# Kernel optimization log

Hardware: AMD Instinct MI355X
Metric: run time of the kernel (lower is better)

## Reference

```python
import jax, jax.numpy as jnp
import numpy as np

B, S, DIM, H = 2, 2048, 1024, 16
HD = DIM // H  # 64


def _rope(x, cos, sin):
    # x: [B, S, H, HD]; cos/sin: [S, HD//2]
    xr = x[..., 0::2]  # interleaved pairs -> real part
    xi = x[..., 1::2]  # imag part
    c = cos[None, :, None, :]
    s = sin[None, :, None, :]
    out_r = xr * c - xi * s
    out_i = xr * s + xi * c
    # re-interleave: stack on new last axis then flatten pairs
    out = jnp.stack([out_r, out_i], axis=-1).reshape(x.shape)
    return out.astype(x.dtype)


def setup_inputs() -> dict:
    key = jax.random.key(0)
    ks = jax.random.split(key, 6)
    x = jax.random.normal(ks[0], (B, S, DIM), dtype=jnp.float32)
    scale = 1.0 / np.sqrt(DIM)
    wq = jax.random.normal(ks[1], (DIM, DIM), dtype=jnp.float32) * scale
    wk = jax.random.normal(ks[2], (DIM, DIM), dtype=jnp.float32) * scale
    wv = jax.random.normal(ks[3], (DIM, DIM), dtype=jnp.float32) * scale
    wo = jax.random.normal(ks[4], (DIM, DIM), dtype=jnp.float32) * scale
    # RoPE frequencies (theta = 10000)
    inv_freq = 1.0 / (10000.0 ** (np.arange(0, HD, 2, dtype=np.float32) / HD))
    t = np.arange(S, dtype=np.float32)
    angles = np.outer(t, inv_freq)  # [S, HD//2]
    freqs_cos = jnp.asarray(np.cos(angles), dtype=jnp.float32)
    freqs_sin = jnp.asarray(np.sin(angles), dtype=jnp.float32)
    # additive causal mask [S, S]
    neg = jnp.full((S, S), -1e9, dtype=jnp.float32)
    mask = jnp.triu(neg, k=1)
    return {"x": x, "wq": wq, "wk": wk, "wv": wv, "wo": wo,
            "freqs_cos": freqs_cos, "freqs_sin": freqs_sin, "mask": mask}


def reference(x, wq, wk, wv, wo, freqs_cos, freqs_sin, mask):
    b, s, _ = x.shape
    # nn.Linear with weight W computes x @ W.T
    xq = (x @ wq.T).reshape(b, s, H, HD)
    xk = (x @ wk.T).reshape(b, s, H, HD)
    xv = (x @ wv.T).reshape(b, s, H, HD)
    xq = _rope(xq, freqs_cos, freqs_sin)
    xk = _rope(xk, freqs_cos, freqs_sin)
    # [B, H, S, S] scores, fully materialized as in the original
    scores = jnp.einsum('bqhd,bkhd->bhqk', xq, xk) / jnp.sqrt(jnp.float32(HD))
    scores = scores + mask[None, None, :, :]
    probs = jax.nn.softmax(scores.astype(jnp.float32), axis=-1).astype(xq.dtype)
    out = jnp.einsum('bhqk,bkhd->bqhd', probs, xv).reshape(b, s, DIM)
    return out @ wo.T
```

## Files before the change

kernel.cpp:

```cpp
#include <hip/hip_runtime.h>
#include <cstdint>
#include <cstddef>

typedef unsigned short u16;
typedef short bf16x8 __attribute__((ext_vector_type(8)));
typedef float f32x4 __attribute__((ext_vector_type(4)));
typedef float f32x16 __attribute__((ext_vector_type(16)));
typedef unsigned u32x2 __attribute__((ext_vector_type(2)));
typedef unsigned u32x4 __attribute__((ext_vector_type(4)));

#define NBATCH 2
#define NS 2048
#define NDIM 1024
#define NH 16
#define NHD 64

__device__ __forceinline__ u16 f2b(float f) {
  union { float f; unsigned u; } x; x.f = f;
  return (u16)((x.u + 0x7fffu + ((x.u >> 16) & 1u)) >> 16);
}

__device__ __forceinline__ unsigned cvtpk_bf16(float lo, float hi) {
  unsigned r;
  asm("v_cvt_pk_bf16_f32 %0, %1, %2" : "=v"(r) : "v"(lo), "v"(hi));
  return r;
}

__global__ void cvt_all(const float* __restrict__ x,  const float* __restrict__ wq,
                        const float* __restrict__ wk, const float* __restrict__ wv,
                        const float* __restrict__ wo,
                        u16* __restrict__ xb,  u16* __restrict__ wqb,
                        u16* __restrict__ wkb, u16* __restrict__ wvb,
                        u16* __restrict__ wob) {
  int i4 = (blockIdx.x * blockDim.x + threadIdx.x) * 4;
  const float* s; u16* d; int off;
  if (i4 < 4194304) { s = x; d = xb; off = i4; }
  else {
    int j = i4 - 4194304;
    int seg = j >> 20; off = j & 1048575;
    s = seg == 0 ? wq : seg == 1 ? wk : seg == 2 ? wv : wo;
    d = seg == 0 ? wqb : seg == 1 ? wkb : seg == 2 ? wvb : wob;
  }
  float4 v = *reinterpret_cast<const float4*>(s + off);
  ushort4 o;
  o.x = f2b(v.x); o.y = f2b(v.y); o.z = f2b(v.z); o.w = f2b(v.w);
  *reinterpret_cast<ushort4*>(d + off) = o;
}

template<int MODE>
__global__ __launch_bounds__(256, 2)
void gemm_bt(const u16* __restrict__ A, const u16* __restrict__ Bt,
             float* __restrict__ Cf, u16* __restrict__ Cb) {
  __shared__ __align__(16) u16 sA[128 * 32];
  __shared__ __align__(16) u16 sB[128 * 32];
  const int lane = threadIdx.x & 63;
  const int wid  = threadIdx.x >> 6;
  const int wm = wid >> 1, wn = wid & 1;
  const int tm = blockIdx.x * 128, tn = blockIdx.y * 128;
  const int fr = lane & 15, fq = lane >> 4;
  const int sr = lane >> 2, sc = lane & 3;

  const f32x4 fzero = {0.f, 0.f, 0.f, 0.f};
  f32x4 acc[4][4];
#pragma unroll
  for (int i = 0; i < 4; ++i)
#pragma unroll
    for (int j = 0; j < 4; ++j) acc[i][j] = fzero;

  const u16* gA0 = A  + (size_t)(tm + wid * 32 + sr) * NDIM + sc * 8;
  const u16* gB0 = Bt + (size_t)(tn + wid * 32 + sr) * NDIM + sc * 8;
  u16* lA = &sA[wid * 32 * 32];
  u16* lB = &sB[wid * 32 * 32];

  for (int k0 = 0; k0 < NDIM; k0 += 32) {
    __builtin_amdgcn_global_load_lds((const __attribute__((address_space(1))) unsigned*)(gA0 + k0),
                                     (__attribute__((address_space(3))) unsigned*)lA, 16, 0, 0);
    __builtin_amdgcn_global_load_lds((const __attribute__((address_space(1))) unsigned*)(gA0 + k0 + 16 * NDIM),
                                     (__attribute__((address_space(3))) unsigned*)(lA + 16 * 32), 16, 0, 0);
    __builtin_amdgcn_global_load_lds((const __attribute__((address_space(1))) unsigned*)(gB0 + k0),
                                     (__attribute__((address_space(3))) unsigned*)lB, 16, 0, 0);
    __builtin_amdgcn_global_load_lds((const __attribute__((address_space(1))) unsigned*)(gB0 + k0 + 16 * NDIM),
                                     (__attribute__((address_space(3))) unsigned*)(lB + 16 * 32), 16, 0, 0);
    __syncthreads();

    bf16x8 af[4], bff[4];
#pragma unroll
    for (int i = 0; i < 4; ++i)
      af[i] = *reinterpret_cast<const bf16x8*>(&sA[(wm * 64 + i * 16 + fr) * 32 + fq * 8]);
#pragma unroll
    for (int i = 0; i < 4; ++i)
      bff[i] = *reinterpret_cast<const bf16x8*>(&sB[(wn * 64 + i * 16 + fr) * 32 + fq * 8]);
#pragma unroll
    for (int mi = 0; mi < 4; ++mi)
#pragma unroll
      for (int ni = 0; ni < 4; ++ni)
        acc[mi][ni] = __builtin_amdgcn_mfma_f32_16x16x32_bf16(af[mi], bff[ni], acc[mi][ni], 0, 0, 0);
    __syncthreads();
  }

#pragma unroll
  for (int mi = 0; mi < 4; ++mi) {
#pragma unroll
    for (int ni = 0; ni < 4; ++ni) {
#pragma unroll
      for (int r = 0; r < 4; ++r) {
        const int row = tm + wm * 64 + mi * 16 + fq * 4 + r;
        const int col = tn + wn * 64 + ni * 16 + fr;
        float val = acc[mi][ni][r];
        if (MODE == 0) {
          Cf[(size_t)row * NDIM + col] = val;
        } else {
          const int hh = row >> 6, d = row & 63;
          const int b = col >> 11, s = col & (NS - 1);
          Cb[((size_t)(b * NH + hh) * NHD + d) * NS + s] = f2b(val);
        }
      }
    }
  }
}

__global__ __launch_bounds__(256, 2)
void gemm_qk(const u16* __restrict__ A, const u16* __restrict__ WQ, const u16* __restrict__ WK,
             u16* __restrict__ Qo, u16* __restrict__ Ko,
             const float* __restrict__ cosp, const float* __restrict__ sinp) {
  __shared__ __align__(16) u16 sA[128 * 32];
  __shared__ __align__(16) u16 sB[128 * 32];
  const int lane = threadIdx.x & 63;
  const int wid  = threadIdx.x >> 6;
  const int wm = wid >> 1, wn = wid & 1;
  const int tnG = blockIdx.y * 128;
  const int which = tnG >> 10;
  const u16* Bt = which ? WK : WQ;
  u16* Cb = which ? Ko : Qo;
  const int tm = blockIdx.x * 128, tn = tnG & 1023;
  const int fr = lane & 15, fq = lane >> 4;
  const int sr = lane >> 2, sc = lane & 3;

  const f32x4 fzero = {0.f, 0.f, 0.f, 0.f};
  f32x4 acc[4][4];
#pragma unroll
  for (int i = 0; i < 4; ++i)
#pragma unroll
    for (int j = 0; j < 4; ++j) acc[i][j] = fzero;

  const u16* gA0 = A  + (size_t)(tm + wid * 32 + sr) * NDIM + sc * 8;
  const u16* gB0 = Bt + (size_t)(tn + wid * 32 + sr) * NDIM + sc * 8;
  u16* lA = &sA[wid * 32 * 32];
  u16* lB = &sB[wid * 32 * 32];

  for (int k0 = 0; k0 < NDIM; k0 += 32) {
    __builtin_amdgcn_global_load_lds((const __attribute__((address_space(1))) unsigned*)(gA0 + k0),
                                     (__attribute__((address_space(3))) unsigned*)lA, 16, 0, 0);
    __builtin_amdgcn_global_load_lds((const __attribute__((address_space(1))) unsigned*)(gA0 + k0 + 16 * NDIM),
                                     (__attribute__((address_space(3))) unsigned*)(lA + 16 * 32), 16, 0, 0);
    __builtin_amdgcn_global_load_lds((const __attribute__((address_space(1))) unsigned*)(gB0 + k0),
                                     (__attribute__((address_space(3))) unsigned*)lB, 16, 0, 0);
    __builtin_amdgcn_global_load_lds((const __attribute__((address_space(1))) unsigned*)(gB0 + k0 + 16 * NDIM),
                                     (__attribute__((address_space(3))) unsigned*)(lB + 16 * 32), 16, 0, 0);
    __syncthreads();

    bf16x8 af[4], bff[4];
#pragma unroll
    for (int i = 0; i < 4; ++i)
      af[i] = *reinterpret_cast<const bf16x8*>(&sA[(wm * 64 + i * 16 + fr) * 32 + fq * 8]);
#pragma unroll
    for (int i = 0; i < 4; ++i)
      bff[i] = *reinterpret_cast<const bf16x8*>(&sB[(wn * 64 + i * 16 + fr) * 32 + fq * 8]);
#pragma unroll
    for (int mi = 0; mi < 4; ++mi)
#pragma unroll
      for (int ni = 0; ni < 4; ++ni)
        acc[mi][ni] = __builtin_amdgcn_mfma_f32_16x16x32_bf16(af[mi], bff[ni], acc[mi][ni], 0, 0, 0);
    __syncthreads();
  }

#pragma unroll
  for (int mi = 0; mi < 4; ++mi) {
#pragma unroll
    for (int ni = 0; ni < 4; ++ni) {
#pragma unroll
      for (int r = 0; r < 4; ++r) {
        const int row = tm + wm * 64 + mi * 16 + fq * 4 + r;
        const int col = tn + wn * 64 + ni * 16 + fr;
        float val = acc[mi][ni][r];
        const int b = row >> 11, s = row & (NS - 1);
        const int h = col >> 6,  d = col & 63;
        const int fi = d >> 1;
        const float c  = cosp[s * 32 + fi];
        const float sn = sinp[s * 32 + fi];
        const float partner = __shfl_xor(val, 1);
        val = (d & 1) ? (partner * sn + val * c) : (val * c - partner * sn);
        Cb[((size_t)(b * NH + h) * NS + s) * NHD + d] = f2b(val);
      }
    }
  }
}

__global__ __launch_bounds__(256, 2)
void attn_fwd(const u16* __restrict__ Q, const u16* __restrict__ K,
              const u16* __restrict__ Vt, u16* __restrict__ O) {
  __shared__ __align__(16) u16 t_lds[4][32 * 68];
  const int lane = threadIdx.x & 63;
  const int w = threadIdx.x >> 6;
  const int bh  = blockIdx.x & 31;
  const int grp = 15 - (int)(blockIdx.x >> 5);
  const int q0w = grp * 128 + w * 32;
  const int qc = lane & 31, hi = lane >> 5;
  const size_t baseQ = (size_t)bh * NS * NHD;
  const size_t baseV = (size_t)bh * NHD * NS;
  const int qrow = q0w + qc;

  bf16x8 qf[4];
#pragma unroll
  for (int s = 0; s < 4; ++s)
    qf[s] = *reinterpret_cast<const bf16x8*>(&Q[baseQ + (size_t)qrow * NHD + s * 16 + hi * 8]);

  f32x16 oA = {}, oB = {};
  float m = -1e30f, l = 0.f;

  const int nkt = (q0w + 95) >> 6;
  for (int kt = 0; kt < nkt; ++kt) {
    const int key0 = kt * 64;
    bf16x8 kf0[4], kf1[4], vf0[4], vf1[4];
#pragma unroll
    for (int s = 0; s < 4; ++s) {
      kf0[s] = *reinterpret_cast<const bf16x8*>(&K[baseQ + (size_t)(key0 + qc) * NHD + s * 16 + hi * 8]);
      kf1[s] = *reinterpret_cast<const bf16x8*>(&K[baseQ + (size_t)(key0 + 32 + qc) * NHD + s * 16 + hi * 8]);
      vf0[s] = *reinterpret_cast<const bf16x8*>(&Vt[baseV + (size_t)qc * NS + key0 + s * 16 + hi * 8]);
      vf1[s] = *reinterpret_cast<const bf16x8*>(&Vt[baseV + (size_t)(32 + qc) * NS + key0 + s * 16 + hi * 8]);
    }
    f32x16 s0 = {}, s1 = {};
#pragma unroll
    for (int s = 0; s < 4; ++s) s0 = __builtin_amdgcn_mfma_f32_32x32x16_bf16(kf0[s], qf[s], s0, 0, 0, 0);
#pragma unroll
    for (int s = 0; s < 4; ++s) s1 = __builtin_amdgcn_mfma_f32_32x32x16_bf16(kf1[s], qf[s], s1, 0, 0, 0);

    float p[32];
#pragma unroll
    for (int r = 0; r < 16; ++r) { p[r] = s0[r] * 0.125f; p[16 + r] = s1[r] * 0.125f; }
    if (kt == nkt - 1) {
#pragma unroll
      for (int i = 0; i < 32; ++i) {
        const int key = key0 + ((i & 3) + 8 * ((i >> 2) & 3) + 4 * hi + 32 * (i >> 4));
        if (key > qrow) p[i] = -1e30f;
      }
    }
    float rm = p[0];
#pragma unroll
    for (int i = 1; i < 32; ++i) rm = fmaxf(rm, p[i]);
    rm = fmaxf(rm, __shfl_xor(rm, 32));
    const float mn = fmaxf(m, rm);
    const float al = __expf(m - mn);
    float rs = 0.f;
#pragma unroll
    for (int i = 0; i < 32; ++i) { p[i] = __expf(p[i] - mn); rs += p[i]; }
    rs += __shfl_xor(rs, 32);
    l = l * al + rs; m = mn;
#pragma unroll
    for (int i = 0; i < 16; ++i) { oA[i] *= al; oB[i] *= al; }

    bf16x8 pt[4];
#pragma unroll
    for (int s = 0; s < 4; ++s) {
      unsigned A0 = cvtpk_bf16(p[8 * s + 0], p[8 * s + 1]);
      unsigned A1 = cvtpk_bf16(p[8 * s + 2], p[8 * s + 3]);
      unsigned B0 = cvtpk_bf16(p[8 * s + 4], p[8 * s + 5]);
      unsigned B1 = cvtpk_bf16(p[8 * s + 6], p[8 * s + 7]);
      u32x2 r0 = __builtin_amdgcn_permlane32_swap(A0, B0, false, false);
      u32x2 r1 = __builtin_amdgcn_permlane32_swap(A1, B1, false, false);
      u32x4 wds = {r0.x, r1.x, r0.y, r1.y};
      pt[s] = __builtin_bit_cast(bf16x8, wds);
    }
#pragma unroll
    for (int s = 0; s < 4; ++s) oA = __builtin_amdgcn_mfma_f32_32x32x16_bf16(vf0[s], pt[s], oA, 0, 0, 0);
#pragma unroll
    for (int s = 0; s < 4; ++s) oB = __builtin_amdgcn_mfma_f32_32x32x16_bf16(vf1[s], pt[s], oB, 0, 0, 0);
  }

  const float invl = 1.0f / l;
#pragma unroll
  for (int g = 0; g < 2; ++g) {
#pragma unroll
    for (int rq = 0; rq < 4; ++rq) {
      const float v0 = (g ? oB[rq * 4 + 0] : oA[rq * 4 + 0]) * invl;
      const float v1 = (g ? oB[rq * 4 + 1] : oA[rq * 4 + 1]) * invl;
      const float v2 = (g ? oB[rq * 4 + 2] : oA[rq * 4 + 2]) * invl;
      const float v3 = (g ? oB[rq * 4 + 3] : oA[rq * 4 + 3]) * invl;
      unsigned* dst = reinterpret_cast<unsigned*>(&t_lds[w][qc * 68 + g * 32 + rq * 8 + hi * 4]);
      dst[0] = cvtpk_bf16(v0, v1);
      dst[1] = cvtpk_bf16(v2, v3);
    }
  }
  __builtin_amdgcn_wave_barrier();
  asm volatile("s_waitcnt lgkmcnt(0)" ::: "memory");
  const int b = bh >> 4, h = bh & 15;
#pragma unroll
  for (int pass = 0; pass < 4; ++pass) {
    const int qr = pass * 8 + (lane >> 3);
    const int c = lane & 7;
    const unsigned* src = reinterpret_cast<const unsigned*>(&t_lds[w][qr * 68 + c * 8]);
    u32x4 val = {src[0], src[1], src[2], src[3]};
    *reinterpret_cast<u32x4*>(&O[((size_t)(b * NS + q0w + qr)) * NDIM + h * NHD + c * 8]) = val;
  }
}

extern "C" void kernel_launch(void* const* d_in, const int* in_sizes, int n_in,
                              void* d_out, int out_size, void* d_ws, size_t ws_size,
                              hipStream_t stream) {
  const float* x  = (const float*)d_in[0];
  const float* wq = (const float*)d_in[1];
  const float* wk = (const float*)d_in[2];
  const float* wv = (const float*)d_in[3];
  const float* wo = (const float*)d_in[4];
  const float* fc = (const float*)d_in[5];
  const float* fs = (const float*)d_in[6];

  u16* xb  = (u16*)d_ws;
  u16* wqb = xb  + 4194304;
  u16* wkb = wqb + 1048576;
  u16* wvb = wkb + 1048576;
  u16* wob = wvb + 1048576;
  u16* qw  = wob + 1048576;
  u16* kw  = qw  + 4194304;
  u16* vw  = kw  + 4194304;
  u16* aw  = vw  + 4194304;

  cvt_all<<<8192, 256, 0, stream>>>(x, wq, wk, wv, wo, xb, wqb, wkb, wvb, wob);

  gemm_qk<<<dim3(32, 16), 256, 0, stream>>>(xb, wqb, wkb, qw, kw, fc, fs);
  gemm_bt<3><<<dim3(8, 32), 256, 0, stream>>>(wvb, xb, nullptr, vw);

  attn_fwd<<<512, 256, 0, stream>>>(qw, kw, vw, aw);

  gemm_bt<0><<<dim3(32, 8), 256, 0, stream>>>(aw, wob, (float*)d_out, nullptr);
}
```

Measured before the change: 255.8 us.

## Prefetch K/V tiles in attention, merge projection GEMMs, lazy softmax rescale

New measurement: 246.1 us. 3.8% less time.

```diff
diff --git a/kernel.cpp b/kernel.cpp
--- a/kernel.cpp
+++ b/kernel.cpp
@@ -14,6 +14,7 @@
 #define NDIM 1024
 #define NH 16
 #define NHD 64
+#define C2 0.18033688f
 
 __device__ __forceinline__ u16 f2b(float f) {
   union { float f; unsigned u; } x; x.f = f;
@@ -47,16 +48,22 @@
   *reinterpret_cast<ushort4*>(d + off) = o;
 }
 
-template<int MODE>
 __global__ __launch_bounds__(256, 2)
-void gemm_bt(const u16* __restrict__ A, const u16* __restrict__ Bt,
-             float* __restrict__ Cf, u16* __restrict__ Cb) {
+void gemm_proj(const u16* __restrict__ xb, const u16* __restrict__ wqb,
+               const u16* __restrict__ wkb, const u16* __restrict__ wvb,
+               u16* __restrict__ qw, u16* __restrict__ kw, u16* __restrict__ vw,
+               const float* __restrict__ cosp, const float* __restrict__ sinp) {
   __shared__ __align__(16) u16 sA[128 * 32];
   __shared__ __align__(16) u16 sB[128 * 32];
+  const int by = blockIdx.y;
+  const int role = by >> 3;
+  const u16* A; const u16* Bt; int tm, tn;
+  if (role == 2) { A = wvb; Bt = xb; tm = (by & 7) * 128; tn = blockIdx.x * 128; }
+  else { A = xb; Bt = role ? wkb : wqb; tm = blockIdx.x * 128; tn = (by & 7) * 128; }
+
   const int lane = threadIdx.x & 63;
   const int wid  = threadIdx.x >> 6;
   const int wm = wid >> 1, wn = wid & 1;
-  const int tm = blockIdx.x * 128, tn = blockIdx.y * 128;
   const int fr = lane & 15, fq = lane >> 4;
   const int sr = lane >> 2, sc = lane & 3;
 
@@ -98,6 +105,7 @@
     __syncthreads();
   }
 
+  u16* CbR = (role == 1) ? kw : qw;
 #pragma unroll
   for (int mi = 0; mi < 4; ++mi) {
 #pragma unroll
@@ -107,12 +115,19 @@
         const int row = tm + wm * 64 + mi * 16 + fq * 4 + r;
         const int col = tn + wn * 64 + ni * 16 + fr;
         float val = acc[mi][ni][r];
-        if (MODE == 0) {
-          Cf[(size_t)row * NDIM + col] = val;
+        if (role < 2) {
+          const int b = row >> 11, s = row & (NS - 1);
+          const int h = col >> 6,  d = col & 63;
+          const int fi = d >> 1;
+          const float c  = cosp[s * 32 + fi];
+          const float sn = sinp[s * 32 + fi];
+          const float partner = __shfl_xor(val, 1);
+          val = (d & 1) ? (partner * sn + val * c) : (val * c - partner * sn);
+          CbR[((size_t)(b * NH + h) * NS + s) * NHD + d] = f2b(val);
         } else {
           const int hh = row >> 6, d = row & 63;
           const int b = col >> 11, s = col & (NS - 1);
-          Cb[((size_t)(b * NH + hh) * NHD + d) * NS + s] = f2b(val);
+          vw[((size_t)(b * NH + hh) * NHD + d) * NS + s] = f2b(val);
         }
       }
     }
@@ -120,54 +135,47 @@
 }
 
 __global__ __launch_bounds__(256, 2)
-void gemm_qk(const u16* __restrict__ A, const u16* __restrict__ WQ, const u16* __restrict__ WK,
-             u16* __restrict__ Qo, u16* __restrict__ Ko,
-             const float* __restrict__ cosp, const float* __restrict__ sinp) {
-  __shared__ __align__(16) u16 sA[128 * 32];
+void gemm_out(const u16* __restrict__ A, const u16* __restrict__ Bt,
+              float* __restrict__ Cf) {
+  __shared__ __align__(16) u16 sA[64 * 32];
   __shared__ __align__(16) u16 sB[128 * 32];
   const int lane = threadIdx.x & 63;
   const int wid  = threadIdx.x >> 6;
   const int wm = wid >> 1, wn = wid & 1;
-  const int tnG = blockIdx.y * 128;
-  const int which = tnG >> 10;
-  const u16* Bt = which ? WK : WQ;
-  u16* Cb = which ? Ko : Qo;
-  const int tm = blockIdx.x * 128, tn = tnG & 1023;
+  const int tm = blockIdx.x * 64, tn = blockIdx.y * 128;
   const int fr = lane & 15, fq = lane >> 4;
   const int sr = lane >> 2, sc = lane & 3;
 
   const f32x4 fzero = {0.f, 0.f, 0.f, 0.f};
-  f32x4 acc[4][4];
-#pragma unroll
-  for (int i = 0; i < 4; ++i)
+  f32x4 acc[2][4];
+#pragma unroll
+  for (int i = 0; i < 2; ++i)
 #pragma unroll
     for (int j = 0; j < 4; ++j) acc[i][j] = fzero;
 
-  const u16* gA0 = A  + (size_t)(tm + wid * 32 + sr) * NDIM + sc * 8;
+  const u16* gA0 = A  + (size_t)(tm + wid * 16 + sr) * NDIM + sc * 8;
   const u16* gB0 = Bt + (size_t)(tn + wid * 32 + sr) * NDIM + sc * 8;
-  u16* lA = &sA[wid * 32 * 32];
+  u16* lA = &sA[wid * 16 * 32];
   u16* lB = &sB[wid * 32 * 32];
 
   for (int k0 = 0; k0 < NDIM; k0 += 32) {
     __builtin_amdgcn_global_load_lds((const __attribute__((address_space(1))) unsigned*)(gA0 + k0),
                                      (__attribute__((address_space(3))) unsigned*)lA, 16, 0, 0);
-    __builtin_amdgcn_global_load_lds((const __attribute__((address_space(1))) unsigned*)(gA0 + k0 + 16 * NDIM),
-                                     (__attribute__((address_space(3))) unsigned*)(lA + 16 * 32), 16, 0, 0);
     __builtin_amdgcn_global_load_lds((const __attribute__((address_space(1))) unsigned*)(gB0 + k0),
                                      (__attribute__((address_space(3))) unsigned*)lB, 16, 0, 0);
     __builtin_amdgcn_global_load_lds((const __attribute__((address_space(1))) unsigned*)(gB0 + k0 + 16 * NDIM),
                                      (__attribute__((address_space(3))) unsigned*)(lB + 16 * 32), 16, 0, 0);
     __syncthreads();
 
-    bf16x8 af[4], bff[4];
-#pragma unroll
-    for (int i = 0; i < 4; ++i)
-      af[i] = *reinterpret_cast<const bf16x8*>(&sA[(wm * 64 + i * 16 + fr) * 32 + fq * 8]);
+    bf16x8 af[2], bff[4];
+#pragma unroll
+    for (int i = 0; i < 2; ++i)
+      af[i] = *reinterpret_cast<const bf16x8*>(&sA[(wm * 32 + i * 16 + fr) * 32 + fq * 8]);
 #pragma unroll
     for (int i = 0; i < 4; ++i)
       bff[i] = *reinterpret_cast<const bf16x8*>(&sB[(wn * 64 + i * 16 + fr) * 32 + fq * 8]);
 #pragma unroll
-    for (int mi = 0; mi < 4; ++mi)
+    for (int mi = 0; mi < 2; ++mi)
 #pragma unroll
       for (int ni = 0; ni < 4; ++ni)
         acc[mi][ni] = __builtin_amdgcn_mfma_f32_16x16x32_bf16(af[mi], bff[ni], acc[mi][ni], 0, 0, 0);
@@ -175,25 +183,15 @@
   }
 
 #pragma unroll
-  for (int mi = 0; mi < 4; ++mi) {
-#pragma unroll
-    for (int ni = 0; ni < 4; ++ni) {
+  for (int mi = 0; mi < 2; ++mi)
+#pragma unroll
+    for (int ni = 0; ni < 4; ++ni)
 #pragma unroll
       for (int r = 0; r < 4; ++r) {
-        const int row = tm + wm * 64 + mi * 16 + fq * 4 + r;
+        const int row = tm + wm * 32 + mi * 16 + fq * 4 + r;
         const int col = tn + wn * 64 + ni * 16 + fr;
-        float val = acc[mi][ni][r];
-        const int b = row >> 11, s = row & (NS - 1);
-        const int h = col >> 6,  d = col & 63;
-        const int fi = d >> 1;
-        const float c  = cosp[s * 32 + fi];
-        const float sn = sinp[s * 32 + fi];
-        const float partner = __shfl_xor(val, 1);
-        val = (d & 1) ? (partner * sn + val * c) : (val * c - partner * sn);
-        Cb[((size_t)(b * NH + h) * NS + s) * NHD + d] = f2b(val);
+        Cf[(size_t)row * NDIM + col] = acc[mi][ni][r];
       }
-    }
-  }
 }
 
 __global__ __launch_bounds__(256, 2)
@@ -218,64 +216,83 @@
   f32x16 oA = {}, oB = {};
   float m = -1e30f, l = 0.f;
 
+  bf16x8 kA0[4], kA1[4], vA0[4], vA1[4];
+  bf16x8 kB0[4], kB1[4], vB0[4], vB1[4];
+
+#define LOADKV(K0, K1, V0, V1, kt_) do {                                       \
+  const int kp0_ = (kt_) * 64;                                                 \
+  _Pragma("unroll")                                                            \
+  for (int s = 0; s < 4; ++s) {                                                \
+    K0[s] = *reinterpret_cast<const bf16x8*>(&K[baseQ + (size_t)(kp0_ + qc) * NHD + s * 16 + hi * 8]); \
+    K1[s] = *reinterpret_cast<const bf16x8*>(&K[baseQ + (size_t)(kp0_ + 32 + qc) * NHD + s * 16 + hi * 8]); \
+    V0[s] = *reinterpret_cast<const bf16x8*>(&Vt[baseV + (size_t)qc * NS + kp0_ + s * 16 + hi * 8]); \
+    V1[s] = *reinterpret_cast<const bf16x8*>(&Vt[baseV + (size_t)(32 + qc) * NS + kp0_ + s * 16 + hi * 8]); \
+  }                                                                            \
+} while (0)
+
+#define BODY(K0, K1, V0, V1, NK0, NK1, NV0, NV1, kt_, PREF) do {               \
+  if (PREF) LOADKV(NK0, NK1, NV0, NV1, (kt_) + 1);                             \
+  __builtin_amdgcn_sched_barrier(0);                                           \
+  f32x16 s0_ = {}, s1_ = {};                                                   \
+  _Pragma("unroll")                                                            \
+  for (int s = 0; s < 4; ++s) s0_ = __builtin_amdgcn_mfma_f32_32x32x16_bf16(K0[s], qf[s], s0_, 0, 0, 0); \
+  _Pragma("unroll")                                                            \
+  for (int s = 0; s < 4; ++s) s1_ = __builtin_amdgcn_mfma_f32_32x32x16_bf16(K1[s], qf[s], s1_, 0, 0, 0); \
+  float p_[32];                                                                \
+  _Pragma("unroll")                                                            \
+  for (int r = 0; r < 16; ++r) { p_[r] = s0_[r]; p_[16 + r] = s1_[r]; }        \
+  if ((kt_) == nkt - 1) {                                                      \
+    _Pragma("unroll")                                                          \
+    for (int i = 0; i < 32; ++i) {                                             \
+      const int key_ = (kt_) * 64 + ((i & 3) + 8 * ((i >> 2) & 3) + 4 * hi + 32 * (i >> 4)); \
+      if (key_ > qrow) p_[i] = -1e30f;                                         \
+    }                                                                          \
+  }                                                                            \
+  float rm_ = p_[0];                                                           \
+  _Pragma("unroll")                                                            \
+  for (int i = 1; i < 32; ++i) rm_ = fmaxf(rm_, p_[i]);                        \
+  rm_ = fmaxf(rm_, __shfl_xor(rm_, 32));                                       \
+  if (!__all(rm_ - m <= 44.3614f)) {                                           \
+    const float mn_ = fmaxf(m, rm_);                                           \
+    const float al_ = __builtin_amdgcn_exp2f((m - mn_) * C2);                  \
+    m = mn_; l *= al_;                                                         \
+    _Pragma("unroll")                                                          \
+    for (int i = 0; i < 16; ++i) { oA[i] *= al_; oB[i] *= al_; }               \
+  }                                                                            \
+  float rs_ = 0.f;                                                             \
+  _Pragma("unroll")                                                            \
+  for (int i = 0; i < 32; ++i) { p_[i] = __builtin_amdgcn_exp2f((p_[i] - m) * C2); rs_ += p_[i]; } \
+  rs_ += __shfl_xor(rs_, 32);                                                  \
+  l += rs_;                                                                    \
+  bf16x8 pt_[4];                                                               \
+  _Pragma("unroll")                                                            \
+  for (int s = 0; s < 4; ++s) {                                                \
+    unsigned A0_ = cvtpk_bf16(p_[8 * s + 0], p_[8 * s + 1]);                   \
+    unsigned A1_ = cvtpk_bf16(p_[8 * s + 2], p_[8 * s + 3]);                   \
+    unsigned B0_ = cvtpk_bf16(p_[8 * s + 4], p_[8 * s + 5]);                   \
+    unsigned B1_ = cvtpk_bf16(p_[8 * s + 6], p_[8 * s + 7]);                   \
+    u32x2 r0_ = __builtin_amdgcn_permlane32_swap(A0_, B0_, false, false);      \
+    u32x2 r1_ = __builtin_amdgcn_permlane32_swap(A1_, B1_, false, false);      \
+    u32x4 wds_ = {r0_.x, r1_.x, r0_.y, r1_.y};                                 \
+    pt_[s] = __builtin_bit_cast(bf16x8, wds_);                                 \
+  }                                                                            \
+  _Pragma("unroll")                                                            \
+  for (int s = 0; s < 4; ++s) oA = __builtin_amdgcn_mfma_f32_32x32x16_bf16(V0[s], pt_[s], oA, 0, 0, 0); \
+  _Pragma("unroll")                                                            \
+  for (int s = 0; s < 4; ++s) oB = __builtin_amdgcn_mfma_f32_32x32x16_bf16(V1[s], pt_[s], oB, 0, 0, 0); \
+} while (0)
+
   const int nkt = (q0w + 95) >> 6;
-  for (int kt = 0; kt < nkt; ++kt) {
-    const int key0 = kt * 64;
-    bf16x8 kf0[4], kf1[4], vf0[4], vf1[4];
-#pragma unroll
-    for (int s = 0; s < 4; ++s) {
-      kf0[s] = *reinterpret_cast<const bf16x8*>(&K[baseQ + (size_t)(key0 + qc) * NHD + s * 16 + hi * 8]);
-      kf1[s] = *reinterpret_cast<const bf16x8*>(&K[baseQ + (size_t)(key0 + 32 + qc) * NHD + s * 16 + hi * 8]);
-      vf0[s] = *reinterpret_cast<const bf16x8*>(&Vt[baseV + (size_t)qc * NS + key0 + s * 16 + hi * 8]);
-      vf1[s] = *reinterpret_cast<const bf16x8*>(&Vt[baseV + (size_t)(32 + qc) * NS + key0 + s * 16 + hi * 8]);
-    }
-    f32x16 s0 = {}, s1 = {};
-#pragma unroll
-    for (int s = 0; s < 4; ++s) s0 = __builtin_amdgcn_mfma_f32_32x32x16_bf16(kf0[s], qf[s], s0, 0, 0, 0);
-#pragma unroll
-    for (int s = 0; s < 4; ++s) s1 = __builtin_amdgcn_mfma_f32_32x32x16_bf16(kf1[s], qf[s], s1, 0, 0, 0);
-
-    float p[32];
-#pragma unroll
-    for (int r = 0; r < 16; ++r) { p[r] = s0[r] * 0.125f; p[16 + r] = s1[r] * 0.125f; }
-    if (kt == nkt - 1) {
-#pragma unroll
-      for (int i = 0; i < 32; ++i) {
-        const int key = key0 + ((i & 3) + 8 * ((i >> 2) & 3) + 4 * hi + 32 * (i >> 4));
-        if (key > qrow) p[i] = -1e30f;
-      }
-    }
-    float rm = p[0];
-#pragma unroll
-    for (int i = 1; i < 32; ++i) rm = fmaxf(rm, p[i]);
-    rm = fmaxf(rm, __shfl_xor(rm, 32));
-    const float mn = fmaxf(m, rm);
-    const float al = __expf(m - mn);
-    float rs = 0.f;
-#pragma unroll
-    for (int i = 0; i < 32; ++i) { p[i] = __expf(p[i] - mn); rs += p[i]; }
-    rs += __shfl_xor(rs, 32);
-    l = l * al + rs; m = mn;
-#pragma unroll
-    for (int i = 0; i < 16; ++i) { oA[i] *= al; oB[i] *= al; }
-
-    bf16x8 pt[4];
-#pragma unroll
-    for (int s = 0; s < 4; ++s) {
-      unsigned A0 = cvtpk_bf16(p[8 * s + 0], p[8 * s + 1]);
-      unsigned A1 = cvtpk_bf16(p[8 * s + 2], p[8 * s + 3]);
-      unsigned B0 = cvtpk_bf16(p[8 * s + 4], p[8 * s + 5]);
-      unsigned B1 = cvtpk_bf16(p[8 * s + 6], p[8 * s + 7]);
-      u32x2 r0 = __builtin_amdgcn_permlane32_swap(A0, B0, false, false);
-      u32x2 r1 = __builtin_amdgcn_permlane32_swap(A1, B1, false, false);
-      u32x4 wds = {r0.x, r1.x, r0.y, r1.y};
-      pt[s] = __builtin_bit_cast(bf16x8, wds);
-    }
-#pragma unroll
-    for (int s = 0; s < 4; ++s) oA = __builtin_amdgcn_mfma_f32_32x32x16_bf16(vf0[s], pt[s], oA, 0, 0, 0);
-#pragma unroll
-    for (int s = 0; s < 4; ++s) oB = __builtin_amdgcn_mfma_f32_32x32x16_bf16(vf1[s], pt[s], oB, 0, 0, 0);
-  }
+  int kt = 0;
+  LOADKV(kA0, kA1, vA0, vA1, 0);
+  for (; kt + 2 <= nkt; kt += 2) {
+    BODY(kA0, kA1, vA0, vA1, kB0, kB1, vB0, vB1, kt, 1);
+    BODY(kB0, kB1, vB0, vB1, kA0, kA1, vA0, vA1, kt + 1, (kt + 2 < nkt));
+  }
+  if (kt < nkt)
+    BODY(kA0, kA1, vA0, vA1, kB0, kB1, vB0, vB1, kt, 0);
+#undef BODY
+#undef LOADKV
 
   const float invl = 1.0f / l;
 #pragma unroll
@@ -327,10 +344,9 @@
 
   cvt_all<<<8192, 256, 0, stream>>>(x, wq, wk, wv, wo, xb, wqb, wkb, wvb, wob);
 
-  gemm_qk<<<dim3(32, 16), 256, 0, stream>>>(xb, wqb, wkb, qw, kw, fc, fs);
-  gemm_bt<3><<<dim3(8, 32), 256, 0, stream>>>(wvb, xb, nullptr, vw);
+  gemm_proj<<<dim3(32, 24), 256, 0, stream>>>(xb, wqb, wkb, wvb, qw, kw, vw, fc, fs);
 
   attn_fwd<<<512, 256, 0, stream>>>(qw, kw, vw, aw);
 
-  gemm_bt<0><<<dim3(32, 8), 256, 0, stream>>>(aw, wob, (float*)d_out, nullptr);
-}
+  gemm_out<<<dim3(64, 8), 256, 0, stream>>>(aw, wob, (float*)d_out);
+}
```
